# Optimization experiments

Measured on AMD Instinct MI355X. Metric: run time of the kernel, lower is better.

## Reference

```python
import jax, jax.numpy as jnp
import numpy as np

N_NODES = 100000

def setup_inputs() -> dict:
    key = jax.random.key(0)
    k1, k2, k3, k4, k5 = jax.random.split(key, 5)
    node_emb = jax.random.normal(k1, (100000, 128), dtype=jnp.float32)
    edge_weight = jax.random.uniform(k2, (1600000,), dtype=jnp.float32)
    src = jax.random.randint(k3, (1600000,), 0, 100000, dtype=jnp.int32)
    dst = jax.random.randint(k4, (1600000,), 0, 100000, dtype=jnp.int32)
    W = jax.random.normal(k5, (128, 128), dtype=jnp.float32) * (1.0 / np.sqrt(128))
    return {"node_emb": node_emb, "edge_weight": edge_weight, "src": src, "dst": dst, "W": W}

def reference(node_emb, edge_weight, src, dst, W):
    # u_mul_e: gather source features, scale by per-edge scalar weight
    msg = node_emb[src] * edge_weight[:, None]          # [E, d]
    # sum reduce into destination nodes (scatter-add / segment-sum)
    agg = jax.ops.segment_sum(msg, dst, num_segments=N_NODES)  # [N, d]
    # linear_out (no bias): agg @ W^T (torch Linear applies x @ W.T)
    return agg @ W.T
```

## Files before the change

kernel.cpp:

```cpp
#include <hip/hip_runtime.h>
#include <cstdint>

typedef unsigned short u16;
typedef unsigned int   u32;

#define DIM     128
#define TPITCH  136
#define BSH     8
#define BSIZE   256
#define NBK_MAX 512
#define CHUNK   4096

__device__ __forceinline__ u16 f2bf(float x) {
    u32 u = __float_as_uint(x);
    u32 r = u + 0x7FFFu + ((u >> 16) & 1u);
    return (u16)(r >> 16);
}

typedef __attribute__((ext_vector_type(8))) short bfrag;
typedef __attribute__((ext_vector_type(4))) float f32x4;
typedef __attribute__((ext_vector_type(2))) float f32x2;

__global__ __launch_bounds__(256) void k_count_transform(
    const float* __restrict__ A, const float* __restrict__ W,
    u16* __restrict__ Tb,
    const int* __restrict__ dst, int* __restrict__ cnt,
    int n, int E, int nCntBlk, int NBK)
{
    __shared__ u16 Wb[DIM * TPITCH];

    if (blockIdx.x < nCntBlk) {
        int* hist = (int*)Wb;
        for (int i = threadIdx.x; i < NBK; i += 256) hist[i] = 0;
        __syncthreads();
        const int base = blockIdx.x * CHUNK;
        const int end  = min(base + CHUNK, E);
        for (int i = base + threadIdx.x; i < end; i += 256)
            atomicAdd(&hist[dst[i] >> BSH], 1);
        __syncthreads();
        for (int b = threadIdx.x; b < NBK; b += 256)
            cnt[b * nCntBlk + blockIdx.x] = hist[b];
        return;
    }

    {
        const int j  = threadIdx.x >> 1;
        const int k0 = (threadIdx.x & 1) << 6;
        const float* wr = W + j * DIM + k0;
        u16* wo = Wb + j * TPITCH + k0;
#pragma unroll
        for (int k = 0; k < 64; k += 4) {
            float4 v = *(const float4*)(wr + k);
            ushort4 h;
            h.x = f2bf(v.x); h.y = f2bf(v.y); h.z = f2bf(v.z); h.w = f2bf(v.w);
            *(ushort4*)(wo + k) = h;
        }
    }
    __syncthreads();

    const int wave = threadIdx.x >> 6;
    const int lane = threadIdx.x & 63;
    const int quad = lane >> 4;
    const int l16  = lane & 15;

    const int r0 = (((blockIdx.x - nCntBlk) << 2) + wave) << 4;
    if (r0 >= n) return;

    const int ar = min(r0 + l16, n - 1);
    const float* arow = A + (size_t)ar * DIM;

    f32x4 acc[8];
#pragma unroll
    for (int c = 0; c < 8; ++c) acc[c] = (f32x4)(0.f);

#pragma unroll
    for (int s = 0; s < 4; ++s) {
        const int koff = (s << 5) + (quad << 3);
        const float4 f0 = *(const float4*)(arow + koff);
        const float4 f1 = *(const float4*)(arow + koff + 4);
        bfrag a;
        a[0] = (short)f2bf(f0.x); a[1] = (short)f2bf(f0.y);
        a[2] = (short)f2bf(f0.z); a[3] = (short)f2bf(f0.w);
        a[4] = (short)f2bf(f1.x); a[5] = (short)f2bf(f1.y);
        a[6] = (short)f2bf(f1.z); a[7] = (short)f2bf(f1.w);
#pragma unroll
        for (int c = 0; c < 8; ++c) {
            const int nn = (c << 4) + l16;
            const bfrag b = *(const bfrag*)(Wb + nn * TPITCH + koff);
            acc[c] = __builtin_amdgcn_mfma_f32_16x16x32_bf16(a, b, acc[c], 0, 0, 0);
        }
    }

#pragma unroll
    for (int r = 0; r < 4; ++r) {
        const int row = r0 + (quad << 2) + r;
        if (row < n) {
            u16* orow = Tb + (size_t)row * DIM + l16;
#pragma unroll
            for (int c = 0; c < 8; ++c)
                orow[c << 4] = f2bf(acc[c][r]);
        }
    }
}

__global__ __launch_bounds__(256) void k_rowsum(
    const int* __restrict__ cnt, int* __restrict__ tot, int nCntBlk)
{
    __shared__ int red[256];
    const int t = threadIdx.x;
    const int* row = cnt + blockIdx.x * nCntBlk;
    int s = 0;
    for (int i = t; i < nCntBlk; i += 256) s += row[i];
    red[t] = s; __syncthreads();
    for (int o = 128; o; o >>= 1) {
        if (t < o) red[t] += red[t + o];
        __syncthreads();
    }
    if (t == 0) tot[blockIdx.x] = red[0];
}

__global__ __launch_bounds__(512) void k_scan_all(
    const int* __restrict__ tot, int* __restrict__ bucketStart,
    int* __restrict__ cnt, int NBK, int nCntBlk, int E)
{
    __shared__ int sc[512];
    __shared__ int bs;
    const int t = threadIdx.x;
    const int b = blockIdx.x;

    const int v = (t < NBK) ? tot[t] : 0;
    sc[t] = v; __syncthreads();
    for (int d = 1; d < 512; d <<= 1) {
        int u = (t >= d) ? sc[t - d] : 0;
        __syncthreads();
        sc[t] += u;
        __syncthreads();
    }
    if (t == b) bs = sc[t] - v;
    if (b == 0) {
        if (t < NBK) bucketStart[t] = sc[t] - v;
        if (t == 0)  bucketStart[NBK] = E;
    }
    __syncthreads();

    int* row = cnt + b * nCntBlk;
    const int rv = (t < nCntBlk) ? row[t] : 0;
    sc[t] = rv; __syncthreads();
    for (int d = 1; d < 512; d <<= 1) {
        int u = (t >= d) ? sc[t - d] : 0;
        __syncthreads();
        sc[t] += u;
        __syncthreads();
    }
    if (t < nCntBlk) row[t] = bs + sc[t] - rv;
}

__global__ __launch_bounds__(512) void k_scatter(
    const int* __restrict__ src, const int* __restrict__ dst,
    const float* __restrict__ w, const int* __restrict__ cnt,
    const int* __restrict__ bucketStart,
    int2* __restrict__ es1, int E, int nCntBlk, int NBK)
{
    __shared__ int2 buf[CHUNK];
    __shared__ u16  bid[CHUNK];
    __shared__ int  gbase[NBK_MAX];
    __shared__ int  lbase[NBK_MAX];
    __shared__ int  lpos[NBK_MAX];
    __shared__ int  sc[512];

    const int blk  = blockIdx.x;
    const int base = blk * CHUNK;
    const int end  = min(base + CHUNK, E);
    const int len  = end - base;
    const int t    = threadIdx.x;

    int mylen = 0;
    if (t < NBK) {
        const int g = cnt[t * nCntBlk + blk];
        gbase[t] = g;
        const int nxt = (blk + 1 < nCntBlk) ? cnt[t * nCntBlk + blk + 1]
                                            : bucketStart[t + 1];
        mylen = nxt - g;
    }
    sc[t] = (t < NBK) ? mylen : 0;
    __syncthreads();
    for (int d = 1; d < 512; d <<= 1) {
        int v = (t >= d) ? sc[t - d] : 0;
        __syncthreads();
        sc[t] += v;
        __syncthreads();
    }
    if (t < NBK) {
        const int ex = sc[t] - mylen;
        lbase[t] = ex;
        lpos[t]  = ex;
    }
    __syncthreads();

    for (int i = base + t; i < end; i += 512) {
        const int d   = dst[i];
        const int bkt = d >> BSH;
        const int p   = atomicAdd(&lpos[bkt], 1);
        buf[p] = make_int2(src[i] | ((d & (BSIZE - 1)) << 20),
                           __float_as_int(w[i]));
        bid[p] = (u16)bkt;
    }
    __syncthreads();

    for (int i = t; i < len; i += 512) {
        const int bkt = bid[i];
        es1[gbase[bkt] + (i - lbase[bkt])] = buf[i];
    }
}

__global__ __launch_bounds__(512) void k_fine(
    const int2* __restrict__ es1, const int* __restrict__ bucketStart,
    int2* __restrict__ es2, int* __restrict__ off, int n, int NBK)
{
    __shared__ int c[BSIZE];
    __shared__ int cur[BSIZE];
    __shared__ int sc[BSIZE];

    const int b = blockIdx.x;
    const int s = bucketStart[b], e = bucketStart[b + 1];
    const int t = threadIdx.x;

    if (t < BSIZE) c[t] = 0;
    __syncthreads();
    for (int i = s + t; i < e; i += 512)
        atomicAdd(&c[es1[i].x >> 20], 1);
    __syncthreads();

    int myc = 0;
    if (t < BSIZE) { myc = c[t]; sc[t] = myc; }
    __syncthreads();
    for (int d = 1; d < BSIZE; d <<= 1) {
        int v = 0;
        if (t < BSIZE && t >= d) v = sc[t - d];
        __syncthreads();
        if (t < BSIZE) sc[t] += v;
        __syncthreads();
    }
    if (t < BSIZE) {
        const int p = s + sc[t] - myc;
        cur[t] = p;
        const int v0 = (b << BSH) + t;
        if (v0 < n) off[v0] = p;
    }
    if (b == NBK - 1 && t == 0) off[n] = e;
    __syncthreads();

    for (int i = s + t; i < e; i += 512) {
        const int2 ev = es1[i];
        const int pp = atomicAdd(&cur[ev.x >> 20], 1);
        es2[pp] = make_int2(ev.x & 0xFFFFF, ev.y);
    }
}

__global__ __launch_bounds__(256) void gnn_aggregate(
    const u16* __restrict__ Tb, const int* __restrict__ off,
    const int2* __restrict__ es, float* __restrict__ out, int n)
{
    const int lane = threadIdx.x & 63;
    const int wv   = threadIdx.x >> 6;
    const u32* Tw  = (const u32*)Tb;
    const int ngrp = (n + 3) >> 2;

    for (int g = blockIdx.x; g < ngrp; g += gridDim.x) {
        const int v = (g << 2) + wv;
        if (v >= n) continue;

        const int b = off[v], e = off[v + 1];
        float ax0 = 0.f, ay0 = 0.f, ax1 = 0.f, ay1 = 0.f;

        int i = b;
        for (; i + 7 < e; i += 8) {
            const int2 e0 = es[i],     e1 = es[i + 1], e2 = es[i + 2], e3 = es[i + 3];
            const int2 e4 = es[i + 4], e5 = es[i + 5], e6 = es[i + 6], e7 = es[i + 7];
            const u32 t0 = Tw[(size_t)e0.x * 64 + lane];
            const u32 t1 = Tw[(size_t)e1.x * 64 + lane];
            const u32 t2 = Tw[(size_t)e2.x * 64 + lane];
            const u32 t3 = Tw[(size_t)e3.x * 64 + lane];
            const u32 t4 = Tw[(size_t)e4.x * 64 + lane];
            const u32 t5 = Tw[(size_t)e5.x * 64 + lane];
            const u32 t6 = Tw[(size_t)e6.x * 64 + lane];
            const u32 t7 = Tw[(size_t)e7.x * 64 + lane];
            const float w0 = __int_as_float(e0.y), w1 = __int_as_float(e1.y);
            const float w2 = __int_as_float(e2.y), w3 = __int_as_float(e3.y);
            const float w4 = __int_as_float(e4.y), w5 = __int_as_float(e5.y);
            const float w6 = __int_as_float(e6.y), w7 = __int_as_float(e7.y);
            ax0 += w0 * __uint_as_float(t0 << 16);
            ay0 += w0 * __uint_as_float(t0 & 0xFFFF0000u);
            ax1 += w1 * __uint_as_float(t1 << 16);
            ay1 += w1 * __uint_as_float(t1 & 0xFFFF0000u);
            ax0 += w2 * __uint_as_float(t2 << 16);
            ay0 += w2 * __uint_as_float(t2 & 0xFFFF0000u);
            ax1 += w3 * __uint_as_float(t3 << 16);
            ay1 += w3 * __uint_as_float(t3 & 0xFFFF0000u);
            ax0 += w4 * __uint_as_float(t4 << 16);
            ay0 += w4 * __uint_as_float(t4 & 0xFFFF0000u);
            ax1 += w5 * __uint_as_float(t5 << 16);
            ay1 += w5 * __uint_as_float(t5 & 0xFFFF0000u);
            ax0 += w6 * __uint_as_float(t6 << 16);
            ay0 += w6 * __uint_as_float(t6 & 0xFFFF0000u);
            ax1 += w7 * __uint_as_float(t7 << 16);
            ay1 += w7 * __uint_as_float(t7 & 0xFFFF0000u);
        }
        for (; i + 3 < e; i += 4) {
            const int2 e0 = es[i], e1 = es[i + 1], e2 = es[i + 2], e3 = es[i + 3];
            const u32 t0 = Tw[(size_t)e0.x * 64 + lane];
            const u32 t1 = Tw[(size_t)e1.x * 64 + lane];
            const u32 t2 = Tw[(size_t)e2.x * 64 + lane];
            const u32 t3 = Tw[(size_t)e3.x * 64 + lane];
            const float w0 = __int_as_float(e0.y), w1 = __int_as_float(e1.y);
            const float w2 = __int_as_float(e2.y), w3 = __int_as_float(e3.y);
            ax0 += w0 * __uint_as_float(t0 << 16);
            ay0 += w0 * __uint_as_float(t0 & 0xFFFF0000u);
            ax1 += w1 * __uint_as_float(t1 << 16);
            ay1 += w1 * __uint_as_float(t1 & 0xFFFF0000u);
            ax0 += w2 * __uint_as_float(t2 << 16);
            ay0 += w2 * __uint_as_float(t2 & 0xFFFF0000u);
            ax1 += w3 * __uint_as_float(t3 << 16);
            ay1 += w3 * __uint_as_float(t3 & 0xFFFF0000u);
        }
        for (; i < e; ++i) {
            const int2 ev = es[i];
            const u32 t = Tw[(size_t)ev.x * 64 + lane];
            const float w0 = __int_as_float(ev.y);
            ax0 += w0 * __uint_as_float(t << 16);
            ay0 += w0 * __uint_as_float(t & 0xFFFF0000u);
        }

        f32x2 r;
        r[0] = ax0 + ax1;
        r[1] = ay0 + ay1;
        __builtin_nontemporal_store(r, (f32x2*)(out + (size_t)v * DIM + 2 * lane));
    }
}

extern "C" void kernel_launch(void* const* d_in, const int* in_sizes, int n_in,
                              void* d_out, int out_size, void* d_ws, size_t ws_size,
                              hipStream_t stream)
{
    const float* node_emb = (const float*)d_in[0];
    const float* ew       = (const float*)d_in[1];
    const int*   src      = (const int*)d_in[2];
    const int*   dst      = (const int*)d_in[3];
    const float* W        = (const float*)d_in[4];
    float* out = (float*)d_out;

    const int n = in_sizes[0] / DIM;
    const int E = in_sizes[1];
    const int NBK = (n + BSIZE - 1) >> BSH;
    const int nCntBlk = (E + CHUNK - 1) / CHUNK;
    const int M = NBK * nCntBlk;

    char* ws = (char*)d_ws;
    size_t o = 0;
    u16* Tb = (u16*)(ws + o);  o += (((size_t)n * DIM * sizeof(u16)) + 255) & ~255ULL;
    int* cnt = (int*)(ws + o); o += (((size_t)M * sizeof(int)) + 255) & ~255ULL;
    int* tot = (int*)(ws + o); o += (((size_t)NBK * sizeof(int)) + 255) & ~255ULL;
    int* bucketStart = (int*)(ws + o); o += (((size_t)(NBK + 1) * sizeof(int)) + 255) & ~255ULL;
    int* off = (int*)(ws + o); o += (((size_t)(n + 1) * sizeof(int)) + 255) & ~255ULL;
    int2* es1 = (int2*)(ws + o); o += (((size_t)E * sizeof(int2)) + 255) & ~255ULL;
    int2* es2 = (int2*)(ws + o);

    const int ntiles = (n + 63) >> 6;

    k_count_transform<<<nCntBlk + ntiles, 256, 0, stream>>>(
        node_emb, W, Tb, dst, cnt, n, E, nCntBlk, NBK);

    k_rowsum<<<NBK, 256, 0, stream>>>(cnt, tot, nCntBlk);
    k_scan_all<<<NBK, 512, 0, stream>>>(tot, bucketStart, cnt, NBK, nCntBlk, E);

    k_scatter<<<nCntBlk, 512, 0, stream>>>(src, dst, ew, cnt, bucketStart,
                                           es1, E, nCntBlk, NBK);

    k_fine<<<NBK, 512, 0, stream>>>(es1, bucketStart, es2, off, n, NBK);

    gnn_aggregate<<<2048, 256, 0, stream>>>(Tb, off, es2, out, n);
}
```

Before: 236.0 us.

## Fuse fine sort into aggregation and use atomic bucket cursors for scatter

Shrinks the coarse bucket size to 64 nodes. Each aggregation block now sorts its bucket's edges in shared memory and aggregates from there, which removes the separate fine-sort kernel, its es2 round trip through global memory, and the off array. The per-block count matrix with its row-sum and scan kernels is replaced by global atomic totals, a single-block scan, and atomic cursor reservation inside the scatter kernel. This drops several launches and global passes, at the cost of nondeterministic edge order within buckets and a slow fallback path for buckets whose edge count exceeds the shared capacity.

```diff
diff --git a/kernel.cpp b/kernel.cpp
--- a/kernel.cpp
+++ b/kernel.cpp
@@ -4,12 +4,14 @@
 typedef unsigned short u16;
 typedef unsigned int   u32;
 
-#define DIM     128
-#define TPITCH  136
-#define BSH     8
-#define BSIZE   256
-#define NBK_MAX 512
-#define CHUNK   4096
+#define DIM      128
+#define TPITCH   136
+#define BSH      6
+#define BSIZE    64
+#define NBK_MAX  1600
+#define CHUNK1   4096
+#define CHUNK3   2048
+#define CAP      1536
 
 __device__ __forceinline__ u16 f2bf(float x) {
     u32 u = __float_as_uint(x);
@@ -21,10 +23,16 @@
 typedef __attribute__((ext_vector_type(4))) float f32x4;
 typedef __attribute__((ext_vector_type(2))) float f32x2;
 
+__global__ __launch_bounds__(256) void k_zero(int* __restrict__ p, int m)
+{
+    const int i = blockIdx.x * 256 + threadIdx.x;
+    if (i < m) p[i] = 0;
+}
+
 __global__ __launch_bounds__(256) void k_count_transform(
     const float* __restrict__ A, const float* __restrict__ W,
     u16* __restrict__ Tb,
-    const int* __restrict__ dst, int* __restrict__ cnt,
+    const int* __restrict__ dst, int* __restrict__ tot,
     int n, int E, int nCntBlk, int NBK)
 {
     __shared__ u16 Wb[DIM * TPITCH];
@@ -33,13 +41,15 @@
         int* hist = (int*)Wb;
         for (int i = threadIdx.x; i < NBK; i += 256) hist[i] = 0;
         __syncthreads();
-        const int base = blockIdx.x * CHUNK;
-        const int end  = min(base + CHUNK, E);
+        const int base = blockIdx.x * CHUNK1;
+        const int end  = min(base + CHUNK1, E);
         for (int i = base + threadIdx.x; i < end; i += 256)
             atomicAdd(&hist[dst[i] >> BSH], 1);
         __syncthreads();
-        for (int b = threadIdx.x; b < NBK; b += 256)
-            cnt[b * nCntBlk + blockIdx.x] = hist[b];
+        for (int b = threadIdx.x; b < NBK; b += 256) {
+            const int h = hist[b];
+            if (h) atomicAdd(&tot[b], h);
+        }
         return;
     }
 
@@ -103,99 +113,84 @@
     }
 }
 
-__global__ __launch_bounds__(256) void k_rowsum(
-    const int* __restrict__ cnt, int* __restrict__ tot, int nCntBlk)
-{
-    __shared__ int red[256];
+__global__ __launch_bounds__(512) void k_scan(
+    const int* __restrict__ tot, int* __restrict__ bucketStart,
+    int* __restrict__ cursor, int NBK, int E)
+{
+    __shared__ int sc[512];
+    __shared__ int carry;
     const int t = threadIdx.x;
-    const int* row = cnt + blockIdx.x * nCntBlk;
-    int s = 0;
-    for (int i = t; i < nCntBlk; i += 256) s += row[i];
-    red[t] = s; __syncthreads();
-    for (int o = 128; o; o >>= 1) {
-        if (t < o) red[t] += red[t + o];
-        __syncthreads();
-    }
-    if (t == 0) tot[blockIdx.x] = red[0];
-}
-
-__global__ __launch_bounds__(512) void k_scan_all(
-    const int* __restrict__ tot, int* __restrict__ bucketStart,
-    int* __restrict__ cnt, int NBK, int nCntBlk, int E)
-{
-    __shared__ int sc[512];
-    __shared__ int bs;
-    const int t = threadIdx.x;
-    const int b = blockIdx.x;
-
-    const int v = (t < NBK) ? tot[t] : 0;
-    sc[t] = v; __syncthreads();
-    for (int d = 1; d < 512; d <<= 1) {
-        int u = (t >= d) ? sc[t - d] : 0;
-        __syncthreads();
-        sc[t] += u;
-        __syncthreads();
-    }
-    if (t == b) bs = sc[t] - v;
-    if (b == 0) {
-        if (t < NBK) bucketStart[t] = sc[t] - v;
-        if (t == 0)  bucketStart[NBK] = E;
-    }
-    __syncthreads();
-
-    int* row = cnt + b * nCntBlk;
-    const int rv = (t < nCntBlk) ? row[t] : 0;
-    sc[t] = rv; __syncthreads();
-    for (int d = 1; d < 512; d <<= 1) {
-        int u = (t >= d) ? sc[t - d] : 0;
-        __syncthreads();
-        sc[t] += u;
-        __syncthreads();
-    }
-    if (t < nCntBlk) row[t] = bs + sc[t] - rv;
+    if (t == 0) carry = 0;
+    __syncthreads();
+
+    for (int c0 = 0; c0 < NBK; c0 += 512) {
+        const int idx = c0 + t;
+        const int v = (idx < NBK) ? tot[idx] : 0;
+        sc[t] = v;
+        __syncthreads();
+        for (int d = 1; d < 512; d <<= 1) {
+            int u = (t >= d) ? sc[t - d] : 0;
+            __syncthreads();
+            sc[t] += u;
+            __syncthreads();
+        }
+        const int excl = carry + sc[t] - v;
+        if (idx < NBK) { bucketStart[idx] = excl; cursor[idx] = excl; }
+        __syncthreads();
+        if (t == 0) carry += sc[511];
+        __syncthreads();
+    }
+    if (t == 0) bucketStart[NBK] = E;
 }
 
 __global__ __launch_bounds__(512) void k_scatter(
     const int* __restrict__ src, const int* __restrict__ dst,
-    const float* __restrict__ w, const int* __restrict__ cnt,
-    const int* __restrict__ bucketStart,
-    int2* __restrict__ es1, int E, int nCntBlk, int NBK)
-{
-    __shared__ int2 buf[CHUNK];
-    __shared__ u16  bid[CHUNK];
-    __shared__ int  gbase[NBK_MAX];
+    const float* __restrict__ w, int* __restrict__ cursor,
+    int2* __restrict__ es1, int E, int NBK)
+{
+    __shared__ int  hist[NBK_MAX];
     __shared__ int  lbase[NBK_MAX];
     __shared__ int  lpos[NBK_MAX];
+    __shared__ int  gbase[NBK_MAX];
+    __shared__ int2 buf[CHUNK3];
+    __shared__ u16  bid[CHUNK3];
     __shared__ int  sc[512];
+    __shared__ int  carry;
 
     const int blk  = blockIdx.x;
-    const int base = blk * CHUNK;
-    const int end  = min(base + CHUNK, E);
+    const int base = blk * CHUNK3;
+    const int end  = min(base + CHUNK3, E);
     const int len  = end - base;
     const int t    = threadIdx.x;
 
-    int mylen = 0;
-    if (t < NBK) {
-        const int g = cnt[t * nCntBlk + blk];
-        gbase[t] = g;
-        const int nxt = (blk + 1 < nCntBlk) ? cnt[t * nCntBlk + blk + 1]
-                                            : bucketStart[t + 1];
-        mylen = nxt - g;
-    }
-    sc[t] = (t < NBK) ? mylen : 0;
-    __syncthreads();
-    for (int d = 1; d < 512; d <<= 1) {
-        int v = (t >= d) ? sc[t - d] : 0;
-        __syncthreads();
-        sc[t] += v;
-        __syncthreads();
-    }
-    if (t < NBK) {
-        const int ex = sc[t] - mylen;
-        lbase[t] = ex;
-        lpos[t]  = ex;
-    }
-    __syncthreads();
+    for (int i = t; i < NBK; i += 512) hist[i] = 0;
+    if (t == 0) carry = 0;
+    __syncthreads();
+    for (int i = base + t; i < end; i += 512)
+        atomicAdd(&hist[dst[i] >> BSH], 1);
+    __syncthreads();
+
+    for (int c0 = 0; c0 < NBK; c0 += 512) {
+        const int idx = c0 + t;
+        const int v = (idx < NBK) ? hist[idx] : 0;
+        sc[t] = v;
+        __syncthreads();
+        for (int d = 1; d < 512; d <<= 1) {
+            int u = (t >= d) ? sc[t - d] : 0;
+            __syncthreads();
+            sc[t] += u;
+            __syncthreads();
+        }
+        const int excl = carry + sc[t] - v;
+        if (idx < NBK) {
+            lbase[idx] = excl;
+            lpos[idx]  = excl;
+            if (v) gbase[idx] = atomicAdd(&cursor[idx], v);
+        }
+        __syncthreads();
+        if (t == 0) carry += sc[511];
+        __syncthreads();
+    }
 
     for (int i = base + t; i < end; i += 512) {
         const int d   = dst[i];
@@ -213,128 +208,143 @@
     }
 }
 
-__global__ __launch_bounds__(512) void k_fine(
-    const int2* __restrict__ es1, const int* __restrict__ bucketStart,
-    int2* __restrict__ es2, int* __restrict__ off, int n, int NBK)
-{
-    __shared__ int c[BSIZE];
-    __shared__ int cur[BSIZE];
-    __shared__ int sc[BSIZE];
-
-    const int b = blockIdx.x;
-    const int s = bucketStart[b], e = bucketStart[b + 1];
-    const int t = threadIdx.x;
-
-    if (t < BSIZE) c[t] = 0;
-    __syncthreads();
-    for (int i = s + t; i < e; i += 512)
-        atomicAdd(&c[es1[i].x >> 20], 1);
-    __syncthreads();
-
-    int myc = 0;
-    if (t < BSIZE) { myc = c[t]; sc[t] = myc; }
-    __syncthreads();
-    for (int d = 1; d < BSIZE; d <<= 1) {
-        int v = 0;
-        if (t < BSIZE && t >= d) v = sc[t - d];
-        __syncthreads();
-        if (t < BSIZE) sc[t] += v;
-        __syncthreads();
-    }
-    if (t < BSIZE) {
-        const int p = s + sc[t] - myc;
-        cur[t] = p;
-        const int v0 = (b << BSH) + t;
-        if (v0 < n) off[v0] = p;
-    }
-    if (b == NBK - 1 && t == 0) off[n] = e;
-    __syncthreads();
-
-    for (int i = s + t; i < e; i += 512) {
-        const int2 ev = es1[i];
-        const int pp = atomicAdd(&cur[ev.x >> 20], 1);
-        es2[pp] = make_int2(ev.x & 0xFFFFF, ev.y);
-    }
-}
-
 __global__ __launch_bounds__(256) void gnn_aggregate(
-    const u16* __restrict__ Tb, const int* __restrict__ off,
-    const int2* __restrict__ es, float* __restrict__ out, int n)
-{
-    const int lane = threadIdx.x & 63;
-    const int wv   = threadIdx.x >> 6;
+    const u16* __restrict__ Tb, const int* __restrict__ bucketStart,
+    const int2* __restrict__ es1, float* __restrict__ out, int n)
+{
+    __shared__ int2 buf[CAP];
+    __shared__ int  cnt[BSIZE];
+    __shared__ int  loff[BSIZE + 1];
+    __shared__ int  cur[BSIZE];
+    __shared__ int  sc64[BSIZE];
+
+    const int b    = blockIdx.x;
+    const int s    = bucketStart[b], e = bucketStart[b + 1];
+    const int len  = e - s;
+    const int v0   = b << BSH;
+    const int t    = threadIdx.x;
+    const int lane = t & 63;
+    const int wv   = t >> 6;
     const u32* Tw  = (const u32*)Tb;
-    const int ngrp = (n + 3) >> 2;
-
-    for (int g = blockIdx.x; g < ngrp; g += gridDim.x) {
-        const int v = (g << 2) + wv;
-        if (v >= n) continue;
-
-        const int b = off[v], e = off[v + 1];
-        float ax0 = 0.f, ay0 = 0.f, ax1 = 0.f, ay1 = 0.f;
-
-        int i = b;
-        for (; i + 7 < e; i += 8) {
-            const int2 e0 = es[i],     e1 = es[i + 1], e2 = es[i + 2], e3 = es[i + 3];
-            const int2 e4 = es[i + 4], e5 = es[i + 5], e6 = es[i + 6], e7 = es[i + 7];
-            const u32 t0 = Tw[(size_t)e0.x * 64 + lane];
-            const u32 t1 = Tw[(size_t)e1.x * 64 + lane];
-            const u32 t2 = Tw[(size_t)e2.x * 64 + lane];
-            const u32 t3 = Tw[(size_t)e3.x * 64 + lane];
-            const u32 t4 = Tw[(size_t)e4.x * 64 + lane];
-            const u32 t5 = Tw[(size_t)e5.x * 64 + lane];
-            const u32 t6 = Tw[(size_t)e6.x * 64 + lane];
-            const u32 t7 = Tw[(size_t)e7.x * 64 + lane];
-            const float w0 = __int_as_float(e0.y), w1 = __int_as_float(e1.y);
-            const float w2 = __int_as_float(e2.y), w3 = __int_as_float(e3.y);
-            const float w4 = __int_as_float(e4.y), w5 = __int_as_float(e5.y);
-            const float w6 = __int_as_float(e6.y), w7 = __int_as_float(e7.y);
-            ax0 += w0 * __uint_as_float(t0 << 16);
-            ay0 += w0 * __uint_as_float(t0 & 0xFFFF0000u);
-            ax1 += w1 * __uint_as_float(t1 << 16);
-            ay1 += w1 * __uint_as_float(t1 & 0xFFFF0000u);
-            ax0 += w2 * __uint_as_float(t2 << 16);
-            ay0 += w2 * __uint_as_float(t2 & 0xFFFF0000u);
-            ax1 += w3 * __uint_as_float(t3 << 16);
-            ay1 += w3 * __uint_as_float(t3 & 0xFFFF0000u);
-            ax0 += w4 * __uint_as_float(t4 << 16);
-            ay0 += w4 * __uint_as_float(t4 & 0xFFFF0000u);
-            ax1 += w5 * __uint_as_float(t5 << 16);
-            ay1 += w5 * __uint_as_float(t5 & 0xFFFF0000u);
-            ax0 += w6 * __uint_as_float(t6 << 16);
-            ay0 += w6 * __uint_as_float(t6 & 0xFFFF0000u);
-            ax1 += w7 * __uint_as_float(t7 << 16);
-            ay1 += w7 * __uint_as_float(t7 & 0xFFFF0000u);
-        }
-        for (; i + 3 < e; i += 4) {
-            const int2 e0 = es[i], e1 = es[i + 1], e2 = es[i + 2], e3 = es[i + 3];
-            const u32 t0 = Tw[(size_t)e0.x * 64 + lane];
-            const u32 t1 = Tw[(size_t)e1.x * 64 + lane];
-            const u32 t2 = Tw[(size_t)e2.x * 64 + lane];
-            const u32 t3 = Tw[(size_t)e3.x * 64 + lane];
-            const float w0 = __int_as_float(e0.y), w1 = __int_as_float(e1.y);
-            const float w2 = __int_as_float(e2.y), w3 = __int_as_float(e3.y);
-            ax0 += w0 * __uint_as_float(t0 << 16);
-            ay0 += w0 * __uint_as_float(t0 & 0xFFFF0000u);
-            ax1 += w1 * __uint_as_float(t1 << 16);
-            ay1 += w1 * __uint_as_float(t1 & 0xFFFF0000u);
-            ax0 += w2 * __uint_as_float(t2 << 16);
-            ay0 += w2 * __uint_as_float(t2 & 0xFFFF0000u);
-            ax1 += w3 * __uint_as_float(t3 << 16);
-            ay1 += w3 * __uint_as_float(t3 & 0xFFFF0000u);
-        }
-        for (; i < e; ++i) {
-            const int2 ev = es[i];
-            const u32 t = Tw[(size_t)ev.x * 64 + lane];
-            const float w0 = __int_as_float(ev.y);
-            ax0 += w0 * __uint_as_float(t << 16);
-            ay0 += w0 * __uint_as_float(t & 0xFFFF0000u);
-        }
-
-        f32x2 r;
-        r[0] = ax0 + ax1;
-        r[1] = ay0 + ay1;
-        __builtin_nontemporal_store(r, (f32x2*)(out + (size_t)v * DIM + 2 * lane));
+
+    if (len <= CAP) {
+        if (t < BSIZE) cnt[t] = 0;
+        __syncthreads();
+        for (int i = s + t; i < e; i += 256)
+            atomicAdd(&cnt[es1[i].x >> 20], 1);
+        __syncthreads();
+
+        int myc = 0;
+        if (t < BSIZE) { myc = cnt[t]; sc64[t] = myc; }
+        __syncthreads();
+        for (int d = 1; d < BSIZE; d <<= 1) {
+            int u = 0;
+            if (t < BSIZE && t >= d) u = sc64[t - d];
+            __syncthreads();
+            if (t < BSIZE) sc64[t] += u;
+            __syncthreads();
+        }
+        if (t < BSIZE) {
+            const int ex = sc64[t] - myc;
+            loff[t] = ex; cur[t] = ex;
+            if (t == BSIZE - 1) loff[BSIZE] = sc64[t];
+        }
+        __syncthreads();
+        for (int i = s + t; i < e; i += 256) {
+            const int2 ev = es1[i];
+            const int p = atomicAdd(&cur[ev.x >> 20], 1);
+            buf[p] = make_int2(ev.x & 0xFFFFF, ev.y);
+        }
+        __syncthreads();
+
+        for (int nt = 0; nt < 16; ++nt) {
+            const int tn = (wv << 4) + nt;
+            const int v  = v0 + tn;
+            if (v >= n) break;
+            const int kb = loff[tn], ke = loff[tn + 1];
+            float ax0 = 0.f, ay0 = 0.f, ax1 = 0.f, ay1 = 0.f;
+
+            int i = kb;
+            for (; i + 7 < ke; i += 8) {
+                const int2 e0 = buf[i],     e1 = buf[i + 1], e2 = buf[i + 2], e3 = buf[i + 3];
+                const int2 e4 = buf[i + 4], e5 = buf[i + 5], e6 = buf[i + 6], e7 = buf[i + 7];
+                const u32 t0 = Tw[(size_t)e0.x * 64 + lane];
+                const u32 t1 = Tw[(size_t)e1.x * 64 + lane];
+                const u32 t2 = Tw[(size_t)e2.x * 64 + lane];
+                const u32 t3 = Tw[(size_t)e3.x * 64 + lane];
+                const u32 t4 = Tw[(size_t)e4.x * 64 + lane];
+                const u32 t5 = Tw[(size_t)e5.x * 64 + lane];
+                const u32 t6 = Tw[(size_t)e6.x * 64 + lane];
+                const u32 t7 = Tw[(size_t)e7.x * 64 + lane];
+                const float w0 = __int_as_float(e0.y), w1 = __int_as_float(e1.y);
+                const float w2 = __int_as_float(e2.y), w3 = __int_as_float(e3.y);
+                const float w4 = __int_as_float(e4.y), w5 = __int_as_float(e5.y);
+                const float w6 = __int_as_float(e6.y), w7 = __int_as_float(e7.y);
+                ax0 += w0 * __uint_as_float(t0 << 16);
+                ay0 += w0 * __uint_as_float(t0 & 0xFFFF0000u);
+                ax1 += w1 * __uint_as_float(t1 << 16);
+                ay1 += w1 * __uint_as_float(t1 & 0xFFFF0000u);
+                ax0 += w2 * __uint_as_float(t2 << 16);
+                ay0 += w2 * __uint_as_float(t2 & 0xFFFF0000u);
+                ax1 += w3 * __uint_as_float(t3 << 16);
+                ay1 += w3 * __uint_as_float(t3 & 0xFFFF0000u);
+                ax0 += w4 * __uint_as_float(t4 << 16);
+                ay0 += w4 * __uint_as_float(t4 & 0xFFFF0000u);
+                ax1 += w5 * __uint_as_float(t5 << 16);
+                ay1 += w5 * __uint_as_float(t5 & 0xFFFF0000u);
+                ax0 += w6 * __uint_as_float(t6 << 16);
+                ay0 += w6 * __uint_as_float(t6 & 0xFFFF0000u);
+                ax1 += w7 * __uint_as_float(t7 << 16);
+                ay1 += w7 * __uint_as_float(t7 & 0xFFFF0000u);
+            }
+            for (; i + 3 < ke; i += 4) {
+                const int2 e0 = buf[i], e1 = buf[i + 1], e2 = buf[i + 2], e3 = buf[i + 3];
+                const u32 t0 = Tw[(size_t)e0.x * 64 + lane];
+                const u32 t1 = Tw[(size_t)e1.x * 64 + lane];
+                const u32 t2 = Tw[(size_t)e2.x * 64 + lane];
+                const u32 t3 = Tw[(size_t)e3.x * 64 + lane];
+                const float w0 = __int_as_float(e0.y), w1 = __int_as_float(e1.y);
+                const float w2 = __int_as_float(e2.y), w3 = __int_as_float(e3.y);
+                ax0 += w0 * __uint_as_float(t0 << 16);
+                ay0 += w0 * __uint_as_float(t0 & 0xFFFF0000u);
+                ax1 += w1 * __uint_as_float(t1 << 16);
+                ay1 += w1 * __uint_as_float(t1 & 0xFFFF0000u);
+                ax0 += w2 * __uint_as_float(t2 << 16);
+                ay0 += w2 * __uint_as_float(t2 & 0xFFFF0000u);
+                ax1 += w3 * __uint_as_float(t3 << 16);
+                ay1 += w3 * __uint_as_float(t3 & 0xFFFF0000u);
+            }
+            for (; i < ke; ++i) {
+                const int2 ev = buf[i];
+                const u32 tv = Tw[(size_t)ev.x * 64 + lane];
+                const float w0 = __int_as_float(ev.y);
+                ax0 += w0 * __uint_as_float(tv << 16);
+                ay0 += w0 * __uint_as_float(tv & 0xFFFF0000u);
+            }
+
+            f32x2 r;
+            r[0] = ax0 + ax1;
+            r[1] = ay0 + ay1;
+            __builtin_nontemporal_store(r, (f32x2*)(out + (size_t)v * DIM + 2 * lane));
+        }
+    } else {
+        for (int nt = 0; nt < 16; ++nt) {
+            const int tn = (wv << 4) + nt;
+            const int v  = v0 + tn;
+            if (v >= n) break;
+            float ax = 0.f, ay = 0.f;
+            for (int i = s; i < e; ++i) {
+                const int2 ev = es1[i];
+                if ((ev.x >> 20) == tn) {
+                    const u32 tv = Tw[(size_t)(ev.x & 0xFFFFF) * 64 + lane];
+                    const float wgt = __int_as_float(ev.y);
+                    ax += wgt * __uint_as_float(tv << 16);
+                    ay += wgt * __uint_as_float(tv & 0xFFFF0000u);
+                }
+            }
+            f32x2 r; r[0] = ax; r[1] = ay;
+            __builtin_nontemporal_store(r, (f32x2*)(out + (size_t)v * DIM + 2 * lane));
+        }
     }
 }
 
@@ -352,31 +362,27 @@
     const int n = in_sizes[0] / DIM;
     const int E = in_sizes[1];
     const int NBK = (n + BSIZE - 1) >> BSH;
-    const int nCntBlk = (E + CHUNK - 1) / CHUNK;
-    const int M = NBK * nCntBlk;
+    const int nCB1 = (E + CHUNK1 - 1) / CHUNK1;
+    const int nCB3 = (E + CHUNK3 - 1) / CHUNK3;
 
     char* ws = (char*)d_ws;
     size_t o = 0;
     u16* Tb = (u16*)(ws + o);  o += (((size_t)n * DIM * sizeof(u16)) + 255) & ~255ULL;
-    int* cnt = (int*)(ws + o); o += (((size_t)M * sizeof(int)) + 255) & ~255ULL;
     int* tot = (int*)(ws + o); o += (((size_t)NBK * sizeof(int)) + 255) & ~255ULL;
     int* bucketStart = (int*)(ws + o); o += (((size_t)(NBK + 1) * sizeof(int)) + 255) & ~255ULL;
-    int* off = (int*)(ws + o); o += (((size_t)(n + 1) * sizeof(int)) + 255) & ~255ULL;
-    int2* es1 = (int2*)(ws + o); o += (((size_t)E * sizeof(int2)) + 255) & ~255ULL;
-    int2* es2 = (int2*)(ws + o);
+    int* cursor = (int*)(ws + o); o += (((size_t)NBK * sizeof(int)) + 255) & ~255ULL;
+    int2* es1 = (int2*)(ws + o);
 
     const int ntiles = (n + 63) >> 6;
 
-    k_count_transform<<<nCntBlk + ntiles, 256, 0, stream>>>(
-        node_emb, W, Tb, dst, cnt, n, E, nCntBlk, NBK);
-
-    k_rowsum<<<NBK, 256, 0, stream>>>(cnt, tot, nCntBlk);
-    k_scan_all<<<NBK, 512, 0, stream>>>(tot, bucketStart, cnt, NBK, nCntBlk, E);
-
-    k_scatter<<<nCntBlk, 512, 0, stream>>>(src, dst, ew, cnt, bucketStart,
-                                           es1, E, nCntBlk, NBK);
-
-    k_fine<<<NBK, 512, 0, stream>>>(es1, bucketStart, es2, off, n, NBK);
-
-    gnn_aggregate<<<2048, 256, 0, stream>>>(Tb, off, es2, out, n);
-}
+    k_zero<<<(NBK + 255) / 256, 256, 0, stream>>>(tot, NBK);
+
+    k_count_transform<<<nCB1 + ntiles, 256, 0, stream>>>(
+        node_emb, W, Tb, dst, tot, n, E, nCB1, NBK);
+
+    k_scan<<<1, 512, 0, stream>>>(tot, bucketStart, cursor, NBK, E);
+
+    k_scatter<<<nCB3, 512, 0, stream>>>(src, dst, ew, cursor, es1, E, NBK);
+
+    gnn_aggregate<<<NBK, 256, 0, stream>>>(Tb, bucketStart, es1, out, n);
+}
```

Measured after the change: 260.3 us. +10.3%, slower.

## Fuse fine-grained destination sort into aggregation via per-block LDS bucketing

Applied to the files above, without the earlier changes.

Removes the separate k_fine kernel and the es2/off global arrays. Each aggregate block now owns 128 destination nodes (half of a coarse bucket). It counts and scans them in LDS, scatters their edges into a shared buffer, then accumulates the bf16 transformed features per node. This saves a global write and re-read of the sorted edge list and one kernel launch. The cost is that each coarse bucket is read twice, once by each half-block. A slow serial fallback runs when a half-bucket exceeds the LDS capacity.

```diff
diff --git a/kernel.cpp b/kernel.cpp
--- a/kernel.cpp
+++ b/kernel.cpp
@@ -10,6 +10,8 @@
 #define BSIZE   256
 #define NBK_MAX 512
 #define CHUNK   4096
+#define FBS     128
+#define CAP     2560
 
 __device__ __forceinline__ u16 f2bf(float x) {
     u32 u = __float_as_uint(x);
@@ -213,128 +215,152 @@
     }
 }
 
-__global__ __launch_bounds__(512) void k_fine(
-    const int2* __restrict__ es1, const int* __restrict__ bucketStart,
-    int2* __restrict__ es2, int* __restrict__ off, int n, int NBK)
-{
-    __shared__ int c[BSIZE];
-    __shared__ int cur[BSIZE];
-    __shared__ int sc[BSIZE];
-
-    const int b = blockIdx.x;
-    const int s = bucketStart[b], e = bucketStart[b + 1];
-    const int t = threadIdx.x;
-
-    if (t < BSIZE) c[t] = 0;
-    __syncthreads();
-    for (int i = s + t; i < e; i += 512)
-        atomicAdd(&c[es1[i].x >> 20], 1);
+__global__ __launch_bounds__(256) void gnn_aggregate(
+    const u16* __restrict__ Tb, const int* __restrict__ bucketStart,
+    const int2* __restrict__ es1, float* __restrict__ out, int n)
+{
+    __shared__ int2 buf[CAP];
+    __shared__ int  cnt[FBS];
+    __shared__ int  loff[FBS + 1];
+    __shared__ int  cur[FBS];
+    __shared__ int  sc[FBS];
+
+    const int f    = blockIdx.x;
+    const int c    = f >> 1;
+    const int hbit = (f & 1) << 7;
+    const int s    = bucketStart[c], e = bucketStart[c + 1];
+    const int v0   = f << 7;
+    const int t    = threadIdx.x;
+    const int lane = t & 63;
+    const int wv   = t >> 6;
+    const u32* Tw  = (const u32*)Tb;
+
+    if (t < FBS) cnt[t] = 0;
+    __syncthreads();
+    for (int i = s + t; i < e; i += 256) {
+        const int d8 = (es1[i].x >> 20) & 255;
+        if ((d8 & 128) == hbit) atomicAdd(&cnt[d8 & 127], 1);
+    }
     __syncthreads();
 
     int myc = 0;
-    if (t < BSIZE) { myc = c[t]; sc[t] = myc; }
-    __syncthreads();
-    for (int d = 1; d < BSIZE; d <<= 1) {
-        int v = 0;
-        if (t < BSIZE && t >= d) v = sc[t - d];
-        __syncthreads();
-        if (t < BSIZE) sc[t] += v;
-        __syncthreads();
-    }
-    if (t < BSIZE) {
-        const int p = s + sc[t] - myc;
-        cur[t] = p;
-        const int v0 = (b << BSH) + t;
-        if (v0 < n) off[v0] = p;
-    }
-    if (b == NBK - 1 && t == 0) off[n] = e;
-    __syncthreads();
-
-    for (int i = s + t; i < e; i += 512) {
-        const int2 ev = es1[i];
-        const int pp = atomicAdd(&cur[ev.x >> 20], 1);
-        es2[pp] = make_int2(ev.x & 0xFFFFF, ev.y);
-    }
-}
-
-__global__ __launch_bounds__(256) void gnn_aggregate(
-    const u16* __restrict__ Tb, const int* __restrict__ off,
-    const int2* __restrict__ es, float* __restrict__ out, int n)
-{
-    const int lane = threadIdx.x & 63;
-    const int wv   = threadIdx.x >> 6;
-    const u32* Tw  = (const u32*)Tb;
-    const int ngrp = (n + 3) >> 2;
-
-    for (int g = blockIdx.x; g < ngrp; g += gridDim.x) {
-        const int v = (g << 2) + wv;
-        if (v >= n) continue;
-
-        const int b = off[v], e = off[v + 1];
-        float ax0 = 0.f, ay0 = 0.f, ax1 = 0.f, ay1 = 0.f;
-
-        int i = b;
-        for (; i + 7 < e; i += 8) {
-            const int2 e0 = es[i],     e1 = es[i + 1], e2 = es[i + 2], e3 = es[i + 3];
-            const int2 e4 = es[i + 4], e5 = es[i + 5], e6 = es[i + 6], e7 = es[i + 7];
-            const u32 t0 = Tw[(size_t)e0.x * 64 + lane];
-            const u32 t1 = Tw[(size_t)e1.x * 64 + lane];
-            const u32 t2 = Tw[(size_t)e2.x * 64 + lane];
-            const u32 t3 = Tw[(size_t)e3.x * 64 + lane];
-            const u32 t4 = Tw[(size_t)e4.x * 64 + lane];
-            const u32 t5 = Tw[(size_t)e5.x * 64 + lane];
-            const u32 t6 = Tw[(size_t)e6.x * 64 + lane];
-            const u32 t7 = Tw[(size_t)e7.x * 64 + lane];
-            const float w0 = __int_as_float(e0.y), w1 = __int_as_float(e1.y);
-            const float w2 = __int_as_float(e2.y), w3 = __int_as_float(e3.y);
-            const float w4 = __int_as_float(e4.y), w5 = __int_as_float(e5.y);
-            const float w6 = __int_as_float(e6.y), w7 = __int_as_float(e7.y);
-            ax0 += w0 * __uint_as_float(t0 << 16);
-            ay0 += w0 * __uint_as_float(t0 & 0xFFFF0000u);
-            ax1 += w1 * __uint_as_float(t1 << 16);
-            ay1 += w1 * __uint_as_float(t1 & 0xFFFF0000u);
-            ax0 += w2 * __uint_as_float(t2 << 16);
-            ay0 += w2 * __uint_as_float(t2 & 0xFFFF0000u);
-            ax1 += w3 * __uint_as_float(t3 << 16);
-            ay1 += w3 * __uint_as_float(t3 & 0xFFFF0000u);
-            ax0 += w4 * __uint_as_float(t4 << 16);
-            ay0 += w4 * __uint_as_float(t4 & 0xFFFF0000u);
-            ax1 += w5 * __uint_as_float(t5 << 16);
-            ay1 += w5 * __uint_as_float(t5 & 0xFFFF0000u);
-            ax0 += w6 * __uint_as_float(t6 << 16);
-            ay0 += w6 * __uint_as_float(t6 & 0xFFFF0000u);
-            ax1 += w7 * __uint_as_float(t7 << 16);
-            ay1 += w7 * __uint_as_float(t7 & 0xFFFF0000u);
-        }
-        for (; i + 3 < e; i += 4) {
-            const int2 e0 = es[i], e1 = es[i + 1], e2 = es[i + 2], e3 = es[i + 3];
-            const u32 t0 = Tw[(size_t)e0.x * 64 + lane];
-            const u32 t1 = Tw[(size_t)e1.x * 64 + lane];
-            const u32 t2 = Tw[(size_t)e2.x * 64 + lane];
-            const u32 t3 = Tw[(size_t)e3.x * 64 + lane];
-            const float w0 = __int_as_float(e0.y), w1 = __int_as_float(e1.y);
-            const float w2 = __int_as_float(e2.y), w3 = __int_as_float(e3.y);
-            ax0 += w0 * __uint_as_float(t0 << 16);
-            ay0 += w0 * __uint_as_float(t0 & 0xFFFF0000u);
-            ax1 += w1 * __uint_as_float(t1 << 16);
-            ay1 += w1 * __uint_as_float(t1 & 0xFFFF0000u);
-            ax0 += w2 * __uint_as_float(t2 << 16);
-            ay0 += w2 * __uint_as_float(t2 & 0xFFFF0000u);
-            ax1 += w3 * __uint_as_float(t3 << 16);
-            ay1 += w3 * __uint_as_float(t3 & 0xFFFF0000u);
-        }
-        for (; i < e; ++i) {
-            const int2 ev = es[i];
-            const u32 t = Tw[(size_t)ev.x * 64 + lane];
-            const float w0 = __int_as_float(ev.y);
-            ax0 += w0 * __uint_as_float(t << 16);
-            ay0 += w0 * __uint_as_float(t & 0xFFFF0000u);
-        }
-
-        f32x2 r;
-        r[0] = ax0 + ax1;
-        r[1] = ay0 + ay1;
-        __builtin_nontemporal_store(r, (f32x2*)(out + (size_t)v * DIM + 2 * lane));
+    if (t < FBS) { myc = cnt[t]; sc[t] = myc; }
+    __syncthreads();
+    for (int d = 1; d < FBS; d <<= 1) {
+        int u = 0;
+        if (t < FBS && t >= d) u = sc[t - d];
+        __syncthreads();
+        if (t < FBS) sc[t] += u;
+        __syncthreads();
+    }
+    if (t < FBS) {
+        const int ex = sc[t] - myc;
+        loff[t] = ex; cur[t] = ex;
+        if (t == FBS - 1) loff[FBS] = sc[t];
+    }
+    __syncthreads();
+    const int kept = loff[FBS];
+
+    if (kept <= CAP) {
+        for (int i = s + t; i < e; i += 256) {
+            const int2 ev = es1[i];
+            const int d8 = (ev.x >> 20) & 255;
+            if ((d8 & 128) == hbit) {
+                const int p = atomicAdd(&cur[d8 & 127], 1);
+                buf[p] = make_int2(ev.x & 0xFFFFF, ev.y);
+            }
+        }
+        __syncthreads();
+
+        for (int nt = 0; nt < 32; ++nt) {
+            const int tn = (wv << 5) + nt;
+            const int v  = v0 + tn;
+            if (v >= n) break;
+            const int kb = loff[tn], ke = loff[tn + 1];
+            float ax0 = 0.f, ay0 = 0.f, ax1 = 0.f, ay1 = 0.f;
+
+            int i = kb;
+            for (; i + 7 < ke; i += 8) {
+                const int2 e0 = buf[i],     e1 = buf[i + 1], e2 = buf[i + 2], e3 = buf[i + 3];
+                const int2 e4 = buf[i + 4], e5 = buf[i + 5], e6 = buf[i + 6], e7 = buf[i + 7];
+                const u32 t0 = Tw[(size_t)e0.x * 64 + lane];
+                const u32 t1 = Tw[(size_t)e1.x * 64 + lane];
+                const u32 t2 = Tw[(size_t)e2.x * 64 + lane];
+                const u32 t3 = Tw[(size_t)e3.x * 64 + lane];
+                const u32 t4 = Tw[(size_t)e4.x * 64 + lane];
+                const u32 t5 = Tw[(size_t)e5.x * 64 + lane];
+                const u32 t6 = Tw[(size_t)e6.x * 64 + lane];
+                const u32 t7 = Tw[(size_t)e7.x * 64 + lane];
+                const float w0 = __int_as_float(e0.y), w1 = __int_as_float(e1.y);
+                const float w2 = __int_as_float(e2.y), w3 = __int_as_float(e3.y);
+                const float w4 = __int_as_float(e4.y), w5 = __int_as_float(e5.y);
+                const float w6 = __int_as_float(e6.y), w7 = __int_as_float(e7.y);
+                ax0 += w0 * __uint_as_float(t0 << 16);
+                ay0 += w0 * __uint_as_float(t0 & 0xFFFF0000u);
+                ax1 += w1 * __uint_as_float(t1 << 16);
+                ay1 += w1 * __uint_as_float(t1 & 0xFFFF0000u);
+                ax0 += w2 * __uint_as_float(t2 << 16);
+                ay0 += w2 * __uint_as_float(t2 & 0xFFFF0000u);
+                ax1 += w3 * __uint_as_float(t3 << 16);
+                ay1 += w3 * __uint_as_float(t3 & 0xFFFF0000u);
+                ax0 += w4 * __uint_as_float(t4 << 16);
+                ay0 += w4 * __uint_as_float(t4 & 0xFFFF0000u);
+                ax1 += w5 * __uint_as_float(t5 << 16);
+                ay1 += w5 * __uint_as_float(t5 & 0xFFFF0000u);
+                ax0 += w6 * __uint_as_float(t6 << 16);
+                ay0 += w6 * __uint_as_float(t6 & 0xFFFF0000u);
+                ax1 += w7 * __uint_as_float(t7 << 16);
+                ay1 += w7 * __uint_as_float(t7 & 0xFFFF0000u);
+            }
+            for (; i + 3 < ke; i += 4) {
+                const int2 e0 = buf[i], e1 = buf[i + 1], e2 = buf[i + 2], e3 = buf[i + 3];
+                const u32 t0 = Tw[(size_t)e0.x * 64 + lane];
+                const u32 t1 = Tw[(size_t)e1.x * 64 + lane];
+                const u32 t2 = Tw[(size_t)e2.x * 64 + lane];
+                const u32 t3 = Tw[(size_t)e3.x * 64 + lane];
+                const float w0 = __int_as_float(e0.y), w1 = __int_as_float(e1.y);
+                const float w2 = __int_as_float(e2.y), w3 = __int_as_float(e3.y);
+                ax0 += w0 * __uint_as_float(t0 << 16);
+                ay0 += w0 * __uint_as_float(t0 & 0xFFFF0000u);
+                ax1 += w1 * __uint_as_float(t1 << 16);
+                ay1 += w1 * __uint_as_float(t1 & 0xFFFF0000u);
+                ax0 += w2 * __uint_as_float(t2 << 16);
+                ay0 += w2 * __uint_as_float(t2 & 0xFFFF0000u);
+                ax1 += w3 * __uint_as_float(t3 << 16);
+                ay1 += w3 * __uint_as_float(t3 & 0xFFFF0000u);
+            }
+            for (; i < ke; ++i) {
+                const int2 ev = buf[i];
+                const u32 tv = Tw[(size_t)ev.x * 64 + lane];
+                const float w0 = __int_as_float(ev.y);
+                ax0 += w0 * __uint_as_float(tv << 16);
+                ay0 += w0 * __uint_as_float(tv & 0xFFFF0000u);
+            }
+
+            f32x2 r;
+            r[0] = ax0 + ax1;
+            r[1] = ay0 + ay1;
+            __builtin_nontemporal_store(r, (f32x2*)(out + (size_t)v * DIM + 2 * lane));
+        }
+    } else {
+        for (int nt = 0; nt < 32; ++nt) {
+            const int tn = (wv << 5) + nt;
+            const int v  = v0 + tn;
+            if (v >= n) break;
+            const int want = hbit | tn;
+            float ax = 0.f, ay = 0.f;
+            for (int i = s; i < e; ++i) {
+                const int2 ev = es1[i];
+                if (((ev.x >> 20) & 255) == want) {
+                    const u32 tv = Tw[(size_t)(ev.x & 0xFFFFF) * 64 + lane];
+                    const float wgt = __int_as_float(ev.y);
+                    ax += wgt * __uint_as_float(tv << 16);
+                    ay += wgt * __uint_as_float(tv & 0xFFFF0000u);
+                }
+            }
+            f32x2 r; r[0] = ax; r[1] = ay;
+            __builtin_nontemporal_store(r, (f32x2*)(out + (size_t)v * DIM + 2 * lane));
+        }
     }
 }
 
@@ -354,6 +380,7 @@
     const int NBK = (n + BSIZE - 1) >> BSH;
     const int nCntBlk = (E + CHUNK - 1) / CHUNK;
     const int M = NBK * nCntBlk;
+    const int nfine = (n + FBS - 1) / FBS;
 
     char* ws = (char*)d_ws;
     size_t o = 0;
@@ -361,9 +388,7 @@
     int* cnt = (int*)(ws + o); o += (((size_t)M * sizeof(int)) + 255) & ~255ULL;
     int* tot = (int*)(ws + o); o += (((size_t)NBK * sizeof(int)) + 255) & ~255ULL;
     int* bucketStart = (int*)(ws + o); o += (((size_t)(NBK + 1) * sizeof(int)) + 255) & ~255ULL;
-    int* off = (int*)(ws + o); o += (((size_t)(n + 1) * sizeof(int)) + 255) & ~255ULL;
-    int2* es1 = (int2*)(ws + o); o += (((size_t)E * sizeof(int2)) + 255) & ~255ULL;
-    int2* es2 = (int2*)(ws + o);
+    int2* es1 = (int2*)(ws + o);
 
     const int ntiles = (n + 63) >> 6;
 
@@ -376,7 +401,5 @@
     k_scatter<<<nCntBlk, 512, 0, stream>>>(src, dst, ew, cnt, bucketStart,
                                            es1, E, nCntBlk, NBK);
 
-    k_fine<<<NBK, 512, 0, stream>>>(es1, bucketStart, es2, off, n, NBK);
-
-    gnn_aggregate<<<2048, 256, 0, stream>>>(Tb, off, es2, out, n);
-}
+    gnn_aggregate<<<nfine, 256, 0, stream>>>(Tb, bucketStart, es1, out, n);
+}
```

Measured after the change: 235.7 us. About the same (-0.1%).
